# Performance work log

Hardware: AMD Instinct MI355X
Metric: run time of the kernel (lower is better)

## Reference

```python
import jax, jax.numpy as jnp
import numpy as np

# HiLo config: dim=384, num_heads=12, alpha=0.5, window_size=2, qkv_bias=False
DIM = 384
N_HEADS = 12
HEAD_DIM = DIM // N_HEADS            # 32
L_HEADS = int(N_HEADS * 0.5)         # 6
H_HEADS = N_HEADS - L_HEADS          # 6
L_DIM = L_HEADS * HEAD_DIM           # 192
H_DIM = H_HEADS * HEAD_DIM           # 192
WS = 2
SCALE = HEAD_DIM ** -0.5
B, H, W = 2, 96, 96


def setup_inputs() -> dict:
    key = jax.random.key(0)
    ks = jax.random.split(key, 8)
    s = 0.02
    return {
        "x": jax.random.normal(ks[0], (B, DIM, H, W), jnp.float32),
        # weights stored [in, out]; linears have no bias except the two proj layers
        "Wh_qkv": jax.random.normal(ks[1], (DIM, H_DIM * 3), jnp.float32) * s,
        "Wh_proj": jax.random.normal(ks[2], (H_DIM, H_DIM), jnp.float32) * s,
        "bh_proj": jnp.zeros((H_DIM,), jnp.float32),
        "Wl_q": jax.random.normal(ks[3], (DIM, L_DIM), jnp.float32) * s,
        "Wl_kv": jax.random.normal(ks[4], (DIM, L_DIM * 2), jnp.float32) * s,
        "Wl_proj": jax.random.normal(ks[5], (L_DIM, L_DIM), jnp.float32) * s,
        "bl_proj": jnp.zeros((L_DIM,), jnp.float32),
    }


def _hifi(x, Wh_qkv, Wh_proj, bh_proj):
    # x: [B, H, W, C] -> windowed local attention over WS x WS windows
    Bx, Hx, Wx, C = x.shape
    hg, wg = Hx // WS, Wx // WS
    G, n = hg * wg, WS * WS
    xw = x.reshape(Bx, hg, WS, wg, WS, C).transpose(0, 1, 3, 2, 4, 5).reshape(Bx, G, n, C)
    qkv = (xw @ Wh_qkv).reshape(Bx, G, n, 3, H_HEADS, HEAD_DIM)
    qkv = qkv.transpose(3, 0, 1, 4, 2, 5)          # [3, B, G, h, n, d]
    q, k, v = qkv[0], qkv[1], qkv[2]
    attn = jnp.einsum('bghnd,bghmd->bghnm', q, k) * SCALE
    attn = jax.nn.softmax(attn, axis=-1)
    out = jnp.einsum('bghnm,bghmd->bghnd', attn, v)  # [B, G, h, n, d]
    out = out.transpose(0, 1, 3, 2, 4).reshape(Bx, hg, wg, WS, WS, H_DIM)
    out = out.transpose(0, 1, 3, 2, 4, 5).reshape(Bx, Hx, Wx, H_DIM)
    return out @ Wh_proj + bh_proj


def _lofi(x, Wl_q, Wl_kv, Wl_proj, bl_proj):
    # x: [B, H, W, C] -> queries from all tokens, K/V from avg-pooled tokens
    Bx, Hx, Wx, C = x.shape
    N = Hx * Wx
    q = (x.reshape(Bx, N, C) @ Wl_q).reshape(Bx, N, L_HEADS, HEAD_DIM).transpose(0, 2, 1, 3)
    # AvgPool2d(WS, WS) on channels-last layout
    xp = x.reshape(Bx, Hx // WS, WS, Wx // WS, WS, C).mean(axis=(2, 4))  # [B, hg, wg, C]
    M = (Hx // WS) * (Wx // WS)
    kv = (xp.reshape(Bx, M, C) @ Wl_kv).reshape(Bx, M, 2, L_HEADS, HEAD_DIM)
    kv = kv.transpose(2, 0, 3, 1, 4)               # [2, B, h, M, d]
    k, v = kv[0], kv[1]
    attn = jnp.einsum('bhnd,bhmd->bhnm', q, k) * SCALE
    attn = jax.nn.softmax(attn, axis=-1)
    out = jnp.einsum('bhnm,bhmd->bhnd', attn, v)   # [B, h, N, d]
    out = out.transpose(0, 2, 1, 3).reshape(Bx, Hx, Wx, L_DIM)
    return out @ Wl_proj + bl_proj


def reference(x, Wh_qkv, Wh_proj, bh_proj, Wl_q, Wl_kv, Wl_proj, bl_proj):
    Bx, C, Hx, Wx = x.shape
    xc = x.transpose(0, 2, 3, 1)                   # [B, H, W, C]
    hi = _hifi(xc, Wh_qkv, Wh_proj, bh_proj)       # [B, H, W, H_DIM]
    lo = _lofi(xc, Wl_q, Wl_kv, Wl_proj, bl_proj)  # [B, H, W, L_DIM]
    out = jnp.concatenate((hi, lo), axis=-1).reshape(Bx, Hx * Wx, C)
    return out.transpose(0, 2, 1).reshape(Bx, C, Hx, Wx)
```

## Files before the change

kernel.cpp:

```cpp
#include <hip/hip_runtime.h>

typedef unsigned short u16;

#define DEV static __device__ __forceinline__

DEV float bf2f(u16 v) { unsigned x = ((unsigned)v) << 16; return __uint_as_float(x); }
DEV u16 f2bf(float f) {
    unsigned x = __float_as_uint(f);
    unsigned r = (x + 0x7fffu + ((x >> 16) & 1u)) >> 16;
    return (u16)r;
}

constexpr int BATCH = 2;
constexpr int CH    = 384;
constexpr int HH    = 96;
constexpr int WW    = 96;
constexpr int NTOK  = HH * WW;
constexpr int GW    = 48;
constexpr int G     = GW * GW;
constexpr int HEADS = 6;
constexpr int NT    = G / 64;
constexpr float SCALE = 0.17677669529663687f;
constexpr float QKSCALE = 0.25503497438034225f;

typedef __attribute__((ext_vector_type(8)))  short short8v;
typedef __attribute__((ext_vector_type(4)))  float f32x4;
typedef __attribute__((ext_vector_type(16))) float f32x16;

DEV f32x4 mfma16(short8v a, short8v b, f32x4 c) {
    return __builtin_amdgcn_mfma_f32_16x16x32_bf16(a, b, c, 0, 0, 0);
}
DEV f32x16 mfma32(short8v a, short8v b, f32x16 c) {
    return __builtin_amdgcn_mfma_f32_32x32x16_bf16(a, b, c, 0, 0, 0);
}

DEV unsigned cvtpk_bf16(float a, float b) {
    unsigned r;
    asm("v_cvt_pk_bf16_f32 %0, %1, %2" : "=v"(r) : "v"(a), "v"(b));
    return r;
}

DEV float exp2fast(float x) {
    float r;
    asm("v_exp_f32 %0, %1" : "=v"(r) : "v"(x));
    return r;
}

DEV float rcpfast(float x) {
    float r;
    asm("v_rcp_f32 %0, %1" : "=v"(r) : "v"(x));
    return r;
}

DEV void permswap(unsigned& a, unsigned& b) {
    asm("v_permlane32_swap_b32 %0, %1" : "+v"(a), "+v"(b));
}

DEV void unpack8(uint4 u, float* f) {
    unsigned a0 = u.x, a1 = u.y, a2 = u.z, a3 = u.w;
    f[0] = bf2f((u16)(a0 & 0xffffu)); f[1] = bf2f((u16)(a0 >> 16));
    f[2] = bf2f((u16)(a1 & 0xffffu)); f[3] = bf2f((u16)(a1 >> 16));
    f[4] = bf2f((u16)(a2 & 0xffffu)); f[5] = bf2f((u16)(a2 >> 16));
    f[6] = bf2f((u16)(a3 & 0xffffu)); f[7] = bf2f((u16)(a3 >> 16));
}

__global__ __launch_bounds__(256) void prep(const float* __restrict__ x,
        const float* __restrict__ W0, const float* __restrict__ W1,
        const float* __restrict__ W2, const float* __restrict__ W3,
        const float* __restrict__ W4,
        u16* __restrict__ xT, u16* __restrict__ xpool,
        u16* __restrict__ D0, u16* __restrict__ D1, u16* __restrict__ D2,
        u16* __restrict__ D3, u16* __restrict__ D4) {
    __shared__ float ts[32][33];
    int tid = threadIdx.x;
    int id = blockIdx.x;
    if (id < 6912) {
        int cx = id % 288, cy = (id / 288) % 12, b = id / 3456;
        int c0 = cx * 32, r0 = cy * 32;
        int row = tid >> 3, cg = tid & 7;
        float4 v = *(const float4*)&x[(size_t)b * CH * NTOK + (size_t)(r0 + row) * NTOK + c0 + cg * 4];
        ts[row][cg * 4 + 0] = v.x; ts[row][cg * 4 + 1] = v.y;
        ts[row][cg * 4 + 2] = v.z; ts[row][cg * 4 + 3] = v.w;
        __syncthreads();
        int cc = tid >> 3, rg = tid & 7;
        uint2 u;
        u.x = (unsigned)f2bf(ts[rg * 4 + 0][cc]) | ((unsigned)f2bf(ts[rg * 4 + 1][cc]) << 16);
        u.y = (unsigned)f2bf(ts[rg * 4 + 2][cc]) | ((unsigned)f2bf(ts[rg * 4 + 3][cc]) << 16);
        *(uint2*)&xT[(size_t)b * NTOK * CH + (size_t)(c0 + cc) * CH + r0 + rg * 4] = u;
    } else if (id < 8640) {
        int t = id - 6912;
        int mx = t % 72, cy = (t / 72) % 12, b = t / 864;
        int m0 = mx * 32, c0 = cy * 32;
        int cc = tid >> 3, mg = tid & 7;
        const float* xb = x + ((size_t)b * CH + c0 + cc) * NTOK;
        #pragma unroll
        for (int i = 0; i < 4; i++) {
            int m = m0 + mg * 4 + i;
            int gy = m / GW, gx = m - gy * GW;
            const float* p = xb + gy * 2 * WW + gx * 2;
            ts[cc][mg * 4 + i] = 0.25f * (p[0] + p[1] + p[WW] + p[WW + 1]);
        }
        __syncthreads();
        int mm = tid >> 3, cg = tid & 7;
        uint2 u;
        u.x = (unsigned)f2bf(ts[cg * 4 + 0][mm]) | ((unsigned)f2bf(ts[cg * 4 + 1][mm]) << 16);
        u.y = (unsigned)f2bf(ts[cg * 4 + 2][mm]) | ((unsigned)f2bf(ts[cg * 4 + 3][mm]) << 16);
        *(uint2*)&xpool[((size_t)b * G + m0 + mm) * CH + c0 + cg * 4] = u;
    } else {
        int wid = id - 8640;
        const float* src; u16* dst; int R, C; float scale; int cx, cy;
        if (wid < 216)      { src = W0; dst = D0; R = 384; C = 576; scale = 1.f;     cx = wid % 18; cy = wid / 18; }
        else if (wid < 288) { src = W1; dst = D1; R = 384; C = 192; scale = QKSCALE; int t = wid - 216; cx = t % 6;  cy = t / 6; }
        else if (wid < 432) { src = W2; dst = D2; R = 384; C = 384; scale = 1.f;     int t = wid - 288; cx = t % 12; cy = t / 12; }
        else if (wid < 468) { src = W3; dst = D3; R = 192; C = 192; scale = 1.f;     int t = wid - 432; cx = t % 6;  cy = t / 6; }
        else                { src = W4; dst = D4; R = 192; C = 192; scale = 1.f;     int t = wid - 468; cx = t % 6;  cy = t / 6; }
        int c0 = cx * 32, r0 = cy * 32;
        int row = tid >> 3, cg = tid & 7;
        float4 v = *(const float4*)&src[(size_t)(r0 + row) * C + c0 + cg * 4];
        ts[row][cg * 4 + 0] = v.x; ts[row][cg * 4 + 1] = v.y;
        ts[row][cg * 4 + 2] = v.z; ts[row][cg * 4 + 3] = v.w;
        __syncthreads();
        int cc = tid >> 3, rg = tid & 7;
        uint2 u;
        u.x = (unsigned)f2bf(scale * ts[rg * 4 + 0][cc]) | ((unsigned)f2bf(scale * ts[rg * 4 + 1][cc]) << 16);
        u.y = (unsigned)f2bf(scale * ts[rg * 4 + 2][cc]) | ((unsigned)f2bf(scale * ts[rg * 4 + 3][cc]) << 16);
        *(uint2*)&dst[(size_t)(c0 + cc) * R + r0 + rg * 4] = u;
    }
}

template<int K>
DEV void gemm64_body(const u16* __restrict__ Pr, const u16* __restrict__ Qr,
                     u16* pt, u16* qt, int tid, f32x4 acc[4]) {
    int w = tid >> 6, lane = tid & 63;
    int l15 = lane & 15, q4 = lane >> 4;
    int lr = tid >> 2, lc = tid & 3;
    const f32x4 zero4 = {0.f, 0.f, 0.f, 0.f};
    acc[0] = zero4; acc[1] = zero4; acc[2] = zero4; acc[3] = zero4;
    uint4 pv = *(const uint4*)&Pr[(size_t)lr * K + lc * 8];
    uint4 qv = *(const uint4*)&Qr[(size_t)lr * K + lc * 8];
    for (int k0 = 0; k0 < K; k0 += 32) {
        __syncthreads();
        *(uint4*)&pt[lr * 40 + lc * 8] = pv;
        *(uint4*)&qt[lr * 40 + lc * 8] = qv;
        if (k0 + 32 < K) {
            pv = *(const uint4*)&Pr[(size_t)lr * K + k0 + 32 + lc * 8];
            qv = *(const uint4*)&Qr[(size_t)lr * K + k0 + 32 + lc * 8];
        }
        __syncthreads();
        short8v pa = *(const short8v*)&pt[(w * 16 + l15) * 40 + q4 * 8];
        #pragma unroll
        for (int qg = 0; qg < 4; qg++) {
            short8v qb = *(const short8v*)&qt[(qg * 16 + l15) * 40 + q4 * 8];
            acc[qg] = mfma16(pa, qb, acc[qg]);
        }
    }
}

__global__ __launch_bounds__(256) void gemm_all(const u16* __restrict__ WT768,
        const u16* __restrict__ xT, const u16* __restrict__ WlkT,
        const u16* __restrict__ WvT, const u16* __restrict__ xpool,
        u16* __restrict__ tokf, u16* __restrict__ kF, u16* __restrict__ vF) {
    __shared__ u16 pt[64 * 40];
    __shared__ u16 qt[64 * 40];
    int tid = threadIdx.x, id = blockIdx.x;
    int w = tid >> 6, lane = tid & 63, l15 = lane & 15, q4 = lane >> 4;
    f32x4 acc[4];
    if (id < 3456) {
        int px = id % 12, qy = (id / 12) % 144, b = id / 1728;
        gemm64_body<CH>(WT768 + (size_t)px * 64 * CH,
                        xT + ((size_t)b * NTOK + qy * 64) * CH, pt, qt, tid, acc);
        #pragma unroll
        for (int qg = 0; qg < 4; qg++) {
            int q = qy * 64 + qg * 16 + l15;
            int p = px * 64 + w * 16 + q4 * 4;
            uint2 pk;
            pk.x = (unsigned)f2bf(acc[qg][0]) | ((unsigned)f2bf(acc[qg][1]) << 16);
            pk.y = (unsigned)f2bf(acc[qg][2]) | ((unsigned)f2bf(acc[qg][3]) << 16);
            *(uint2*)&tokf[((size_t)b * NTOK + q) * 768 + p] = pk;
        }
    } else if (id < 3672) {
        int u = id - 3456;
        int px = u % 3, qy = (u / 3) % 36, b = u / 108;
        gemm64_body<CH>(WlkT + (size_t)px * 64 * CH,
                        xpool + ((size_t)b * G + qy * 64) * CH, pt, qt, tid, acc);
        #pragma unroll
        for (int qg = 0; qg < 4; qg++) {
            int m = qy * 64 + qg * 16 + l15;
            int d = px * 64 + w * 16 + q4 * 4;
            int h = d >> 5, dh = (d >> 4) & 1, hi2 = (d >> 3) & 1;
            int kh = (m >> 5) & 1, tile = m >> 6, slot = kh * 2 + dh;
            int lane2 = (m & 31) + 32 * hi2;
            size_t addr = ((((size_t)(b * HEADS + h) * NT + tile) * 4 + slot) * 64 + lane2) * 8 + (d & 7);
            uint2 pk;
            pk.x = (unsigned)f2bf(acc[qg][0]) | ((unsigned)f2bf(acc[qg][1]) << 16);
            pk.y = (unsigned)f2bf(acc[qg][2]) | ((unsigned)f2bf(acc[qg][3]) << 16);
            *(uint2*)&kF[addr] = pk;
        }
    } else {
        int u = id - 3672;
        int px = u % 36, qy = (u / 36) % 3, b = u / 108;
        gemm64_body<CH>(xpool + ((size_t)b * G + px * 64) * CH,
                        WvT + (size_t)qy * 64 * CH, pt, qt, tid, acc);
        #pragma unroll
        for (int qg = 0; qg < 4; qg++) {
            int jj = qy * 64 + qg * 16 + l15;
            int m = px * 64 + w * 16 + q4 * 4;
            int h = jj >> 5, d31 = jj & 31;
            int tile = m >> 6, slot = (m >> 4) & 3, hi2 = (m >> 3) & 1;
            int lane2 = d31 + 32 * hi2;
            size_t addr = ((((size_t)(b * HEADS + h) * NT + tile) * 4 + slot) * 64 + lane2) * 8 + (m & 7);
            uint2 pk;
            pk.x = (unsigned)f2bf(acc[qg][0]) | ((unsigned)f2bf(acc[qg][1]) << 16);
            pk.y = (unsigned)f2bf(acc[qg][2]) | ((unsigned)f2bf(acc[qg][3]) << 16);
            *(uint2*)&vF[addr] = pk;
        }
    }
}

__global__ __launch_bounds__(256, 4) void mega_attn(const u16* __restrict__ tokf,
        const u16* __restrict__ kF, const u16* __restrict__ vF,
        u16* __restrict__ hi_ao, u16* __restrict__ lo_ao) {
    __shared__ float smem[3168];
    int tid = threadIdx.x;
    int grp = blockIdx.x / 7, rem = blockIdx.x % 7;
    const f32x16 zero16 = {0.f,0.f,0.f,0.f,0.f,0.f,0.f,0.f,0.f,0.f,0.f,0.f,0.f,0.f,0.f,0.f};

    if (rem < 3) {
        int lid = grp * 3 + rem;
        int lane = tid & 63, kq = tid >> 6;
        int l31 = lane & 31, hi = lane >> 5;
        int qt = lid % 288, h = (lid / 288) % HEADS, b = lid / 1728;

        const short8v ones = {(short)0x3F80, (short)0x3F80, (short)0x3F80, (short)0x3F80,
                              (short)0x3F80, (short)0x3F80, (short)0x3F80, (short)0x3F80};

        short8v qb0, qb1;
        {
            int nq = qt * 32 + l31;
            const u16* qrow = &tokf[((size_t)b * NTOK + nq) * 768 + 576 + h * 32];
            qb0 = *(const short8v*)&qrow[hi * 8];
            qb1 = *(const short8v*)&qrow[16 + hi * 8];
        }
        f32x16 accO = zero16, accL = zero16;

        const u16* kp = kF + ((size_t)(b * HEADS + h) * NT + kq * 9) * 2048 + lane * 8;
        const u16* vp = vF + ((size_t)(b * HEADS + h) * NT + kq * 9) * 2048 + lane * 8;

        for (int t = 0; t < 9; t++) {
            short8v kb0 = *(const short8v*)(kp);
            short8v kb1 = *(const short8v*)(kp + 512);
            short8v kb2 = *(const short8v*)(kp + 1024);
            short8v kb3 = *(const short8v*)(kp + 1536);
            short8v vb0 = *(const short8v*)(vp);
            short8v vb1 = *(const short8v*)(vp + 512);
            short8v vb2 = *(const short8v*)(vp + 1024);
            short8v vb3 = *(const short8v*)(vp + 1536);
            kp += 2048; vp += 2048;

            f32x16 s0 = mfma32(kb0, qb0, zero16);
            s0 = mfma32(kb1, qb1, s0);
            unsigned pk0[8];
            #pragma unroll
            for (int i = 0; i < 8; i++)
                pk0[i] = cvtpk_bf16(exp2fast(s0[2 * i]), exp2fast(s0[2 * i + 1]));
            permswap(pk0[0], pk0[2]);
            permswap(pk0[1], pk0[3]);
            permswap(pk0[4], pk0[6]);
            permswap(pk0[5], pk0[7]);

            f32x16 s1 = mfma32(kb2, qb0, zero16);
            s1 = mfma32(kb3, qb1, s1);
            unsigned pk1[8];
            #pragma unroll
            for (int i = 0; i < 8; i++)
                pk1[i] = cvtpk_bf16(exp2fast(s1[2 * i]), exp2fast(s1[2 * i + 1]));
            permswap(pk1[0], pk1[2]);
            permswap(pk1[1], pk1[3]);
            permswap(pk1[4], pk1[6]);
            permswap(pk1[5], pk1[7]);

            union { unsigned u[4]; short8v v; } pa;
            pa.u[0] = pk0[0]; pa.u[1] = pk0[1]; pa.u[2] = pk0[2]; pa.u[3] = pk0[3];
            accO = mfma32(pa.v, vb0, accO);
            accL = mfma32(pa.v, ones, accL);
            pa.u[0] = pk0[4]; pa.u[1] = pk0[5]; pa.u[2] = pk0[6]; pa.u[3] = pk0[7];
            accO = mfma32(pa.v, vb1, accO);
            accL = mfma32(pa.v, ones, accL);
            pa.u[0] = pk1[0]; pa.u[1] = pk1[1]; pa.u[2] = pk1[2]; pa.u[3] = pk1[3];
            accO = mfma32(pa.v, vb2, accO);
            accL = mfma32(pa.v, ones, accL);
            pa.u[0] = pk1[4]; pa.u[1] = pk1[5]; pa.u[2] = pk1[6]; pa.u[3] = pk1[7];
            accO = mfma32(pa.v, vb3, accO);
            accL = mfma32(pa.v, ones, accL);
        }

        float* mO = smem;
        float* mL = smem + 3072;
        if (kq) {
            int base = (kq - 1) * 1024;
            #pragma unroll
            for (int r = 0; r < 16; r++) mO[base + r * 64 + lane] = accO[r];
            if (l31 == 0) {
                #pragma unroll
                for (int r = 0; r < 16; r++) mL[(kq - 1) * 32 + hi * 16 + r] = accL[r];
            }
        }
        __syncthreads();
        if (kq == 0) {
            #pragma unroll
            for (int w2 = 0; w2 < 3; w2++) {
                int base = w2 * 1024;
                #pragma unroll
                for (int r = 0; r < 16; r++) {
                    accO[r] += mO[base + r * 64 + lane];
                    accL[r] += mL[w2 * 32 + hi * 16 + r];
                }
            }
            #pragma unroll
            for (int r = 0; r < 16; r++) {
                int qr = (r & 3) + 8 * (r >> 2) + 4 * hi;
                int n = qt * 32 + qr;
                lo_ao[((size_t)b * NTOK + n) * 192 + h * 32 + l31] =
                    f2bf(accO[r] * rcpfast(accL[r]));
            }
        }
    } else {
        int bg = grp * 4 + (rem - 3);
        int b = bg / G, g = bg % G;
        int gy = g / GW, gx = g % GW;
        float (*sq)[576] = (float(*)[576])smem;
        float* satt = smem + 2304;
        float* sp   = smem + 2400;

        for (int c = tid; c < 288; c += 256) {
            int t = c / 72, j8 = c - t * 72;
            int n = (gy * 2 + (t >> 1)) * WW + gx * 2 + (t & 1);
            uint4 u = *(const uint4*)&tokf[((size_t)b * NTOK + n) * 768 + j8 * 8];
            unpack8(u, &sq[t][j8 * 8]);
        }
        __syncthreads();

        if (tid < 96) {
            int h = tid >> 4, tq = (tid >> 2) & 3, tm = tid & 3;
            const float* qp = &sq[tq][h * 32];
            const float* kp = &sq[tm][192 + h * 32];
            float s0 = 0, s1 = 0, s2 = 0, s3 = 0;
            #pragma unroll
            for (int d = 0; d < 32; d += 4) {
                s0 += qp[d] * kp[d];
                s1 += qp[d + 1] * kp[d + 1];
                s2 += qp[d + 2] * kp[d + 2];
                s3 += qp[d + 3] * kp[d + 3];
            }
            satt[h * 16 + tq * 4 + tm] = (s0 + s1 + s2 + s3) * SCALE;
        }
        __syncthreads();
        if (tid < 24) {
            int h = tid >> 2, t = tid & 3;
            float l0 = satt[h * 16 + t * 4 + 0], l1 = satt[h * 16 + t * 4 + 1];
            float l2 = satt[h * 16 + t * 4 + 2], l3 = satt[h * 16 + t * 4 + 3];
            float mx = fmaxf(fmaxf(l0, l1), fmaxf(l2, l3));
            float e0 = __expf(l0 - mx), e1 = __expf(l1 - mx);
            float e2 = __expf(l2 - mx), e3 = __expf(l3 - mx);
            float inv = 1.0f / (e0 + e1 + e2 + e3);
            sp[h * 16 + t * 4 + 0] = e0 * inv; sp[h * 16 + t * 4 + 1] = e1 * inv;
            sp[h * 16 + t * 4 + 2] = e2 * inv; sp[h * 16 + t * 4 + 3] = e3 * inv;
        }
        __syncthreads();
        {
            int t = tid >> 6, hp = (tid >> 5) & 1, d = tid & 31;
            int n = (gy * 2 + (t >> 1)) * WW + gx * 2 + (t & 1);
            u16* op = &hi_ao[((size_t)b * NTOK + n) * 192];
            #pragma unroll
            for (int hh = 0; hh < 3; hh++) {
                int h = hp * 3 + hh;
                float o = sp[h * 16 + t * 4 + 0] * sq[0][384 + h * 32 + d]
                        + sp[h * 16 + t * 4 + 1] * sq[1][384 + h * 32 + d]
                        + sp[h * 16 + t * 4 + 2] * sq[2][384 + h * 32 + d]
                        + sp[h * 16 + t * 4 + 3] * sq[3][384 + h * 32 + d];
                op[h * 32 + d] = f2bf(o);
            }
        }
    }
}

__global__ __launch_bounds__(256) void proj_both(const u16* __restrict__ hi_ao,
        const u16* __restrict__ lo_ao, const u16* __restrict__ WhpT,
        const u16* __restrict__ WlpT, const float* __restrict__ bh,
        const float* __restrict__ bl, float* __restrict__ out) {
    __shared__ u16 pt[64 * 40];
    __shared__ u16 qt[64 * 40];
    int tid = threadIdx.x;
    int z = blockIdx.z, which = z >> 1, b = z & 1;
    const u16* A = which ? lo_ao : hi_ao;
    const u16* W = which ? WlpT : WhpT;
    const float* bias = which ? bl : bh;
    int p0 = blockIdx.x * 64, q0 = blockIdx.y * 64;
    f32x4 acc[4];
    gemm64_body<192>(A + ((size_t)b * NTOK + p0) * 192, W + (size_t)q0 * 192,
                     pt, qt, tid, acc);
    int w = tid >> 6, lane = tid & 63, l15 = lane & 15, q4 = lane >> 4;
    #pragma unroll
    for (int qg = 0; qg < 4; qg++) {
        int q = q0 + qg * 16 + l15;
        int p = p0 + w * 16 + q4 * 4;
        float bb = bias[q];
        float4 o = make_float4(acc[qg][0] + bb, acc[qg][1] + bb,
                               acc[qg][2] + bb, acc[qg][3] + bb);
        *(float4*)&out[((size_t)b * CH + which * 192 + q) * NTOK + p] = o;
    }
}

extern "C" void kernel_launch(void* const* d_in, const int* in_sizes, int n_in,
                              void* d_out, int out_size, void* d_ws, size_t ws_size,
                              hipStream_t stream) {
    const float* x       = (const float*)d_in[0];
    const float* Wh_qkv  = (const float*)d_in[1];
    const float* Wh_proj = (const float*)d_in[2];
    const float* bh_proj = (const float*)d_in[3];
    const float* Wl_q    = (const float*)d_in[4];
    const float* Wl_kv   = (const float*)d_in[5];
    const float* Wl_proj = (const float*)d_in[6];
    const float* bl_proj = (const float*)d_in[7];
    float* out = (float*)d_out;

    char* ws = (char*)d_ws;
    u16*   tokf  = (u16*)ws;
    char*  ws1   = ws + (size_t)28311552;
    u16*   xT    = (u16*)ws1;
    u16*   hi_ao = (u16*)ws1;
    u16*   lo_ao = (u16*)(ws1 + 7077888);
    char*  ws2   = ws1 + (size_t)14155776;
    u16*   kF    = (u16*)ws2;
    u16*   vF    = (u16*)(ws2 + 1769472);
    char*  ws3   = ws2 + (size_t)7077888;
    u16*   xpool = (u16*)ws3;
    char*  ws4   = ws3 + (size_t)3538944;
    u16*   WT768 = (u16*)ws4;
    u16*   WlkvT = WT768 + 768 * 384;
    u16*   WhpT  = WlkvT + 384 * 384;
    u16*   WlpT  = WhpT + 192 * 192;
    u16*   WlkT  = WlkvT;
    u16*   WvT   = WlkvT + 192 * 384;

    prep<<<dim3(9144), 256, 0, stream>>>(
        x, Wh_qkv, Wl_q, Wl_kv, Wh_proj, Wl_proj,
        xT, xpool, WT768, WT768 + 576 * 384, WlkvT, WhpT, WlpT);

    gemm_all<<<dim3(3888), 256, 0, stream>>>(
        WT768, xT, WlkT, WvT, xpool, tokf, kF, vF);

    mega_attn<<<dim3(8064), 256, 0, stream>>>(tokf, kF, vF, hi_ao, lo_ao);

    proj_both<<<dim3(144, 3, 4), 256, 0, stream>>>(
        hi_ao, lo_ao, WhpT, WlpT, bh_proj, bl_proj, out);
}
```

Baseline: 125.9 us.

## Share K/V tiles in LDS across four query waves in lofi attention

The lofi attention block now has its four waves handle four different 32-query tiles, 128 queries per block. They share each K/V tile, which is loaded cooperatively into LDS with a register prefetch of the next tile. Previously the four waves split the key range for one 32-query tile and then reduced partial accumulators through shared memory. The change cuts global K/V traffic by 4x and removes the cross-wave reduction, at the cost of two barriers per key tile. The grid is regrouped from 7 to 19 blocks per group (3 lofi, 16 hifi) and shared memory shrinks.

```diff
diff --git a/kernel.cpp b/kernel.cpp
--- a/kernel.cpp
+++ b/kernel.cpp
@@ -220,42 +220,55 @@
 __global__ __launch_bounds__(256, 4) void mega_attn(const u16* __restrict__ tokf,
         const u16* __restrict__ kF, const u16* __restrict__ vF,
         u16* __restrict__ hi_ao, u16* __restrict__ lo_ao) {
-    __shared__ float smem[3168];
+    __shared__ float smem[2560];
     int tid = threadIdx.x;
-    int grp = blockIdx.x / 7, rem = blockIdx.x % 7;
+    int grp = blockIdx.x / 19, rem = blockIdx.x % 19;
     const f32x16 zero16 = {0.f,0.f,0.f,0.f,0.f,0.f,0.f,0.f,0.f,0.f,0.f,0.f,0.f,0.f,0.f,0.f};
 
     if (rem < 3) {
         int lid = grp * 3 + rem;
-        int lane = tid & 63, kq = tid >> 6;
+        int lane = tid & 63, w = tid >> 6;
         int l31 = lane & 31, hi = lane >> 5;
-        int qt = lid % 288, h = (lid / 288) % HEADS, b = lid / 1728;
+        int qt = lid % 72, h = (lid / 72) % HEADS, b = lid / 432;
 
         const short8v ones = {(short)0x3F80, (short)0x3F80, (short)0x3F80, (short)0x3F80,
                               (short)0x3F80, (short)0x3F80, (short)0x3F80, (short)0x3F80};
 
         short8v qb0, qb1;
         {
-            int nq = qt * 32 + l31;
+            int nq = qt * 128 + w * 32 + l31;
             const u16* qrow = &tokf[((size_t)b * NTOK + nq) * 768 + 576 + h * 32];
             qb0 = *(const short8v*)&qrow[hi * 8];
             qb1 = *(const short8v*)&qrow[16 + hi * 8];
         }
         f32x16 accO = zero16, accL = zero16;
 
-        const u16* kp = kF + ((size_t)(b * HEADS + h) * NT + kq * 9) * 2048 + lane * 8;
-        const u16* vp = vF + ((size_t)(b * HEADS + h) * NT + kq * 9) * 2048 + lane * 8;
-
-        for (int t = 0; t < 9; t++) {
-            short8v kb0 = *(const short8v*)(kp);
-            short8v kb1 = *(const short8v*)(kp + 512);
-            short8v kb2 = *(const short8v*)(kp + 1024);
-            short8v kb3 = *(const short8v*)(kp + 1536);
-            short8v vb0 = *(const short8v*)(vp);
-            short8v vb1 = *(const short8v*)(vp + 512);
-            short8v vb2 = *(const short8v*)(vp + 1024);
-            short8v vb3 = *(const short8v*)(vp + 1536);
-            kp += 2048; vp += 2048;
+        const u16* kbase = kF + ((size_t)(b * HEADS + h) * NT) * 2048 + tid * 8;
+        const u16* vbase = vF + ((size_t)(b * HEADS + h) * NT) * 2048 + tid * 8;
+        u16* skl = (u16*)smem;
+        u16* svl = skl + 2048;
+
+        uint4 kreg = *(const uint4*)kbase;
+        uint4 vreg = *(const uint4*)vbase;
+
+        for (int t = 0; t < NT; t++) {
+            __syncthreads();
+            *(uint4*)&skl[tid * 8] = kreg;
+            *(uint4*)&svl[tid * 8] = vreg;
+            if (t + 1 < NT) {
+                kreg = *(const uint4*)(kbase + (size_t)(t + 1) * 2048);
+                vreg = *(const uint4*)(vbase + (size_t)(t + 1) * 2048);
+            }
+            __syncthreads();
+
+            short8v kb0 = *(const short8v*)&skl[lane * 8];
+            short8v kb1 = *(const short8v*)&skl[512 + lane * 8];
+            short8v kb2 = *(const short8v*)&skl[1024 + lane * 8];
+            short8v kb3 = *(const short8v*)&skl[1536 + lane * 8];
+            short8v vb0 = *(const short8v*)&svl[lane * 8];
+            short8v vb1 = *(const short8v*)&svl[512 + lane * 8];
+            short8v vb2 = *(const short8v*)&svl[1024 + lane * 8];
+            short8v vb3 = *(const short8v*)&svl[1536 + lane * 8];
 
             f32x16 s0 = mfma32(kb0, qb0, zero16);
             s0 = mfma32(kb1, qb1, s0);
@@ -294,38 +307,15 @@
             accL = mfma32(pa.v, ones, accL);
         }
 
-        float* mO = smem;
-        float* mL = smem + 3072;
-        if (kq) {
-            int base = (kq - 1) * 1024;
-            #pragma unroll
-            for (int r = 0; r < 16; r++) mO[base + r * 64 + lane] = accO[r];
-            if (l31 == 0) {
-                #pragma unroll
-                for (int r = 0; r < 16; r++) mL[(kq - 1) * 32 + hi * 16 + r] = accL[r];
-            }
-        }
-        __syncthreads();
-        if (kq == 0) {
-            #pragma unroll
-            for (int w2 = 0; w2 < 3; w2++) {
-                int base = w2 * 1024;
-                #pragma unroll
-                for (int r = 0; r < 16; r++) {
-                    accO[r] += mO[base + r * 64 + lane];
-                    accL[r] += mL[w2 * 32 + hi * 16 + r];
-                }
-            }
-            #pragma unroll
-            for (int r = 0; r < 16; r++) {
-                int qr = (r & 3) + 8 * (r >> 2) + 4 * hi;
-                int n = qt * 32 + qr;
-                lo_ao[((size_t)b * NTOK + n) * 192 + h * 32 + l31] =
-                    f2bf(accO[r] * rcpfast(accL[r]));
-            }
+        #pragma unroll
+        for (int r = 0; r < 16; r++) {
+            int qr = (r & 3) + 8 * (r >> 2) + 4 * hi;
+            int n = qt * 128 + w * 32 + qr;
+            lo_ao[((size_t)b * NTOK + n) * 192 + h * 32 + l31] =
+                f2bf(accO[r] * rcpfast(accL[r]));
         }
     } else {
-        int bg = grp * 4 + (rem - 3);
+        int bg = grp * 16 + (rem - 3);
         int b = bg / G, g = bg % G;
         int gy = g / GW, gx = g % GW;
         float (*sq)[576] = (float(*)[576])smem;
@@ -450,7 +440,7 @@
     gemm_all<<<dim3(3888), 256, 0, stream>>>(
         WT768, xT, WlkT, WvT, xpool, tokf, kF, vF);
 
-    mega_attn<<<dim3(8064), 256, 0, stream>>>(tokf, kF, vF, hi_ao, lo_ao);
+    mega_attn<<<dim3(5472), 256, 0, stream>>>(tokf, kF, vF, hi_ao, lo_ao);
 
     proj_both<<<dim3(144, 3, 4), 256, 0, stream>>>(
         hi_ao, lo_ao, WhpT, WlpT, bh_proj, bl_proj, out);
```

Result: slower. 131.6 us (+4.5%).
